# Kernel tuning notes

Measured on AMD Instinct MI355X. Metric: run time of the kernel, lower is better.

The kernel has to match this reference:

```python
import jax, jax.numpy as jnp
import numpy as np

B, N, R, T, E, H, FE = 2, 512, 64, 128, 64, 8, 4
D = E // H  # head_dim = 8


def _layernorm(x, g, b):
    m = x.mean(-1, keepdims=True)
    v = ((x - m) ** 2).mean(-1, keepdims=True)
    return (x - m) / jnp.sqrt(v + 1e-5) * g + b


def _sattn(v, k, q, Wv, Wk, Wq, Wo, bo, mask):
    # v,k: (Bk,Nk,T,E); q: (Bq,Nq,T,E) with Bq possibly 1 (broadcast on batch)
    Bk, Nk, Tk, _ = v.shape
    Nq = q.shape[1]
    v = v.reshape(Bk, Nk, Tk, H, D) @ Wv
    k = k.reshape(Bk, Nk, Tk, H, D) @ Wk
    q = q.reshape(q.shape[0], Nq, Tk, H, D) @ Wq
    q = jnp.broadcast_to(q, (Bk, Nq, Tk, H, D))
    energy = jnp.einsum('bqthd,bkthd->bqkth', q, k)  # (B,Nq,Nk,T,H)
    if mask is not None:
        m = mask[None, :, :, None, None]
        energy = energy * m + (-1e8) * (1.0 - m)
    # note: non-standard softmax over the QUERY axis (dim=1), after scale+clamp
    att = jax.nn.softmax(jnp.clip(energy * (float(E) ** -0.5), -5.0, 5.0), axis=1)
    out = jnp.einsum('bqkth,bkthd->bqthd', att, v).reshape(Bk, Nq, Tk, E)
    return out @ Wo + bo, att


def setup_inputs() -> dict:
    rng = jax.random.key(0)
    ks = jax.random.split(rng, 40)
    s = 0.05
    inp = {
        'value': jax.random.normal(ks[0], (B, N, T, E), jnp.float32),
        'key': jax.random.normal(ks[1], (B, N, T, E), jnp.float32),
        'query': jax.random.normal(ks[2], (B, N, T, E), jnp.float32),
        'adj_sr': jax.random.randint(ks[3], (N, R), 0, 2).astype(jnp.int32),
        'adj_r': jax.random.randint(ks[4], (R, R), 0, 2).astype(jnp.int32),
        'D_S': jax.random.normal(ks[5], (N, R), jnp.float32) * s,
        'W_emb': jax.random.normal(ks[6], (R, E), jnp.float32) * s,
        'b_emb': jnp.zeros((E,), jnp.float32),
        'I_param': jax.random.normal(ks[7], (R, 1, E), jnp.float32) * s,
        'g1': jnp.ones((E,), jnp.float32), 'beta1': jnp.zeros((E,), jnp.float32),
        'g2': jnp.ones((E,), jnp.float32), 'beta2': jnp.zeros((E,), jnp.float32),
        'W_ff1': jax.random.normal(ks[8], (E, FE * E), jnp.float32) * s,
        'b_ff1': jnp.zeros((FE * E,), jnp.float32),
        'W_ff2': jax.random.normal(ks[9], (FE * E, E), jnp.float32) * s,
        'b_ff2': jnp.zeros((E,), jnp.float32),
        'W_fs': jax.random.normal(ks[10], (E, E), jnp.float32) * s,
        'b_fs': jnp.zeros((E,), jnp.float32),
    }
    i = 11
    for tag in ('sr', 'rr', 'rs'):
        inp['Wv_' + tag] = jax.random.normal(ks[i + 0], (D, D), jnp.float32) * s
        inp['Wk_' + tag] = jax.random.normal(ks[i + 1], (D, D), jnp.float32) * s
        inp['Wq_' + tag] = jax.random.normal(ks[i + 2], (D, D), jnp.float32) * s
        inp['Wo_' + tag] = jax.random.normal(ks[i + 3], (E, E), jnp.float32) * s
        inp['bo_' + tag] = jnp.zeros((E,), jnp.float32)
        i += 4
    return inp


def reference(value, key, query, adj_sr, adj_r, D_S, W_emb, b_emb, I_param,
              g1, beta1, g2, beta2, W_ff1, b_ff1, W_ff2, b_ff2, W_fs, b_fs,
              Wv_sr, Wk_sr, Wq_sr, Wo_sr, bo_sr,
              Wv_rr, Wk_rr, Wq_rr, Wo_rr, bo_rr,
              Wv_rs, Wk_rs, Wq_rs, Wo_rs, bo_rs):
    m_sr = adj_sr.T.astype(jnp.float32)  # (R,N)
    m_r = adj_r.astype(jnp.float32)      # (R,R)
    ds = D_S @ W_emb + b_emb             # (N,E)
    q = query + ds[None, :, None, :]
    k = key + ds[None, :, None, :]
    v = value
    Iq = jnp.broadcast_to(I_param[None], (1, R, T, E))  # I.repeat(1,1,T,1)
    Hh, asr = _sattn(v, k, Iq, Wv_sr, Wk_sr, Wq_sr, Wo_sr, bo_sr, m_sr)
    Hh, arr = _sattn(Hh, Hh, Hh, Wv_rr, Wk_rr, Wq_rr, Wo_rr, bo_rr, m_r)
    attn, ars = _sattn(Hh, Hh, q, Wv_rs, Wk_rs, Wq_rs, Wo_rs, bo_rs, None)
    x = _layernorm(attn + q, g1, beta1)          # dropout=0.0 -> identity
    ff = jax.nn.relu(x @ W_ff1 + b_ff1) @ W_ff2 + b_ff2
    U = _layernorm(ff + x, g2, beta2)
    out = U @ W_fs + b_fs
    return (out, asr, arr, ars, Hh)
```

## Files before the change

### kernel.cpp

```cpp
#include <hip/hip_runtime.h>
#include <hip/hip_bf16.h>

typedef __hip_bfloat16 bf16;

#define Bc 2
#define Nc 512
#define Rc 64
#define Tc 128
#define Ec 64
#define Hc 8
#define THc 1024
#define FFc 256

__device__ __forceinline__ bf16  f2b(float x){ return __float2bfloat16(x); }
__device__ __forceinline__ float us2f(unsigned short u){
  union { unsigned int i; float f; } c; c.i = ((unsigned int)u) << 16; return c.f;
}
__device__ __forceinline__ float clip5(float x){ return fminf(fmaxf(x, -5.0f), 5.0f); }

__device__ __forceinline__ float wave_sum64(float v){
#pragma unroll
  for (int o = 32; o > 0; o >>= 1) v += __shfl_xor(v, o, 64);
  return v;
}
__device__ __forceinline__ void wave_sum64x2(float& a, float& b){
#pragma unroll
  for (int o = 32; o > 0; o >>= 1){
    a += __shfl_xor(a, o, 64);
    b += __shfl_xor(b, o, 64);
  }
}
__device__ __forceinline__ void wave_sum64x4(float& a, float& b, float& c, float& d){
#pragma unroll
  for (int o = 32; o > 0; o >>= 1){
    a += __shfl_xor(a, o, 64);
    b += __shfl_xor(b, o, 64);
    c += __shfl_xor(c, o, 64);
    d += __shfl_xor(d, o, 64);
  }
}

__device__ __forceinline__ float rowred16_sum(float v){
  v += __shfl_xor(v, 1, 64);
  v += __shfl_xor(v, 2, 64);
  v += __shfl_xor(v, 4, 64);
  v += __shfl_xor(v, 8, 64);
  return v;
}

__global__ __launch_bounds__(64) void k_prep(
    const float* __restrict__ DS, const float* __restrict__ Wemb,
    const float* __restrict__ bemb, const float* __restrict__ Ip,
    const float* __restrict__ Wq, float* __restrict__ ds, float* __restrict__ qhat)
{
  int bid = blockIdx.x, t = threadIdx.x;
  if (bid < Nc){
    int n = bid, e = t;
    __shared__ float row[Rc];
    row[t] = DS[n*Rc + t];
    __syncthreads();
    float acc = bemb[e];
    for (int r = 0; r < Rc; ++r) acc += row[r] * Wemb[r*Ec + e];
    ds[n*Ec + e] = acc;
  } else {
    int r = bid - Nc;
    __shared__ float irow[Ec];
    irow[t] = Ip[r*Ec + t];
    __syncthreads();
    int h = t >> 3, d = t & 7;
    float acc = 0.0f;
#pragma unroll
    for (int d0 = 0; d0 < 8; ++d0) acc += irow[h*8 + d0] * Wq[d0*8 + d];
    qhat[r*Ec + h*8 + d] = acc;
  }
}

__global__ __launch_bounds__(256) void k_proj_sr(
    const float* __restrict__ key, const float* __restrict__ value,
    const float* __restrict__ ds, const float* __restrict__ Wk,
    const float* __restrict__ Wv, float* __restrict__ khat, float* __restrict__ vhat)
{
  __shared__ float wk[64], wv[64];
  int t = threadIdx.x;
  if (t < 64){ wk[t] = Wk[t]; wv[t] = Wv[t]; }
  __syncthreads();
  int u = blockIdx.x*256 + t;
  int h = u & 7;
  int nt = u >> 3;
  int n = (nt / Tc) % Nc;
  const float* kp = key + (size_t)u*8;
  const float* vp = value + (size_t)u*8;
  const float* dsp = ds + n*Ec + h*8;
  float kin[8], vin[8];
#pragma unroll
  for (int d = 0; d < 8; ++d){ kin[d] = kp[d] + dsp[d]; vin[d] = vp[d]; }
  float* ko = khat + (size_t)u*8;
  float* vo = vhat + (size_t)u*8;
#pragma unroll
  for (int d = 0; d < 8; ++d){
    float ka = 0.0f, va = 0.0f;
#pragma unroll
    for (int d0 = 0; d0 < 8; ++d0){ ka += kin[d0]*wk[d0*8+d]; va += vin[d0]*wv[d0*8+d]; }
    ko[d] = ka; vo[d] = va;
  }
}

__global__ __launch_bounds__(256) void k_asr_write(
    const float* __restrict__ khat, const float* __restrict__ qhat,
    const int* __restrict__ adj_sr, float* __restrict__ o_asr,
    float* __restrict__ rDsr)
{
  __shared__ float ql[4096];
  const float EXPM5 = 0.006737946999085467f;
  int bid = blockIdx.x;
  int b = bid >> 8, np = bid & 255;
  int tid = threadIdx.x;
  int n = np*2 + (tid >> 7);
  int t = tid & 127;
#pragma unroll
  for (int i = 0; i < 16; ++i) ql[i*256 + tid] = qhat[i*256 + tid];
  __syncthreads();
  const float* kp = khat + ((size_t)((b*Nc + n)*Tc + t))*Ec;
  float kr[64];
#pragma unroll
  for (int i = 0; i < 16; ++i) *(float4*)&kr[i*4] = *(const float4*)&kp[i*4];

  float s[8] = {0,0,0,0,0,0,0,0};
  for (int r = 0; r < 64; ++r){
    int m = adj_sr[n*Rc + r];
    if (m){
      const float* qr = &ql[r*64];
#pragma unroll
      for (int h = 0; h < 8; ++h){
        float4 qa = *(const float4*)&qr[h*8];
        float4 qb = *(const float4*)&qr[h*8 + 4];
        float e = qa.x*kr[h*8+0] + qa.y*kr[h*8+1] + qa.z*kr[h*8+2] + qa.w*kr[h*8+3]
                + qb.x*kr[h*8+4] + qb.y*kr[h*8+5] + qb.z*kr[h*8+6] + qb.w*kr[h*8+7];
        s[h] += __expf(clip5(e*0.125f));
      }
    } else {
#pragma unroll
      for (int h = 0; h < 8; ++h) s[h] += EXPM5;
    }
  }
  float rs_[8];
#pragma unroll
  for (int h = 0; h < 8; ++h) rs_[h] = __builtin_amdgcn_rcpf(s[h]);
  {
    size_t dbase = ((size_t)((b*Nc + n)*Tc + t))*8;
    *(float4*)&rDsr[dbase]     = make_float4(rs_[0], rs_[1], rs_[2], rs_[3]);
    *(float4*)&rDsr[dbase + 4] = make_float4(rs_[4], rs_[5], rs_[6], rs_[7]);
  }

  for (int r = 0; r < 64; ++r){
    int m = adj_sr[n*Rc + r];
    float a[8];
    if (m){
      const float* qr = &ql[r*64];
#pragma unroll
      for (int h = 0; h < 8; ++h){
        float4 qa = *(const float4*)&qr[h*8];
        float4 qb = *(const float4*)&qr[h*8 + 4];
        float e = qa.x*kr[h*8+0] + qa.y*kr[h*8+1] + qa.z*kr[h*8+2] + qa.w*kr[h*8+3]
                + qb.x*kr[h*8+4] + qb.y*kr[h*8+5] + qb.z*kr[h*8+6] + qb.w*kr[h*8+7];
        a[h] = __expf(clip5(e*0.125f)) * rs_[h];
      }
    } else {
#pragma unroll
      for (int h = 0; h < 8; ++h) a[h] = EXPM5 * rs_[h];
    }
    size_t ao = ((size_t)((b*Rc + r)*Nc + n))*THc + t*8;
    *(float4*)&o_asr[ao]     = make_float4(a[0], a[1], a[2], a[3]);
    *(float4*)&o_asr[ao + 4] = make_float4(a[4], a[5], a[6], a[7]);
  }
}

__global__ __launch_bounds__(256) void k_attn_sr(
    const float* __restrict__ khat, const float* __restrict__ vhat,
    const float* __restrict__ qhat, const int* __restrict__ adj_sr,
    const float* __restrict__ rD, float* __restrict__ pre)
{
  __shared__ float accs[4][64][8];
  __shared__ float rDl[512];
  int bid = blockIdx.x;
  int b = bid >> 10, th = bid & 1023;
  int t = th >> 3, h = th & 7;
  int tid = threadIdx.x;
  int r = tid & 63, w = tid >> 6;
  rDl[tid]       = rD[((size_t)((b*Nc + tid      )*Tc + t))*8 + h];
  rDl[tid + 256] = rD[((size_t)((b*Nc + tid + 256)*Tc + t))*8 + h];
  float q[8];
#pragma unroll
  for (int d = 0; d < 8; ++d) q[d] = qhat[r*Ec + h*8 + d];
  __syncthreads();
  float acc[8] = {0,0,0,0,0,0,0,0};
  int n0 = w*128;
  for (int n = n0; n < n0 + 128; n += 2){
    size_t goA = ((size_t)((b*Nc + n)*Tc + t))*Ec + h*8;
    size_t goB = goA + (size_t)Tc*Ec;
    const float* kA = khat + goA;
    const float* kB = khat + goB;
    float eA = 0.0f, eB = 0.0f;
#pragma unroll
    for (int d = 0; d < 8; ++d){ eA += q[d]*kA[d]; eB += q[d]*kB[d]; }
    int mA = adj_sr[n*Rc + r], mB = adj_sr[(n+1)*Rc + r];
    eA = mA ? clip5(eA*0.125f) : -5.0f;
    eB = mB ? clip5(eB*0.125f) : -5.0f;
    float aA = __expf(eA) * rDl[n];
    float aB = __expf(eB) * rDl[n+1];
    const float* vA = vhat + goA;
    const float* vB = vhat + goB;
#pragma unroll
    for (int d = 0; d < 8; ++d) acc[d] += aA*vA[d] + aB*vB[d];
  }
#pragma unroll
  for (int d = 0; d < 8; ++d) accs[w][r][d] = acc[d];
  __syncthreads();
  if (w == 0){
    size_t po = ((size_t)((b*Rc + r)*Tc + t))*Ec + h*8;
#pragma unroll
    for (int d = 0; d < 8; ++d)
      pre[po + d] = accs[0][r][d] + accs[1][r][d] + accs[2][r][d] + accs[3][r][d];
  }
}

__global__ __launch_bounds__(256) void k_attn_rr(
    const float* __restrict__ qh, const float* __restrict__ kh,
    const float* __restrict__ vh, const int* __restrict__ adj_r,
    bf16* __restrict__ att_c, float* __restrict__ pre)
{
  __shared__ float accs[4][64][8];
  int bid = blockIdx.x;
  int b = bid >> 10, th = bid & 1023;
  int t = th >> 3, h = th & 7;
  int tid = threadIdx.x;
  int q = tid & 63, w = tid >> 6;
  size_t qo = ((size_t)((b*Rc + q)*Tc + t))*Ec + h*8;
  float qv[8];
#pragma unroll
  for (int d = 0; d < 8; ++d) qv[d] = qh[qo + d];
  float acc[8] = {0,0,0,0,0,0,0,0};
  int k0 = w*16;
  for (int k = k0; k < k0 + 16; k += 2){
    size_t koA = ((size_t)((b*Rc + k)*Tc + t))*Ec + h*8;
    size_t koB = koA + (size_t)Tc*Ec;
    const float* kA = kh + koA;
    const float* kB = kh + koB;
    float eA = 0.0f, eB = 0.0f;
#pragma unroll
    for (int d = 0; d < 8; ++d){ eA += qv[d]*kA[d]; eB += qv[d]*kB[d]; }
    int mA = adj_r[q*Rc + k], mB = adj_r[q*Rc + k + 1];
    eA = mA ? clip5(eA*0.125f) : -5.0f;
    eB = mB ? clip5(eB*0.125f) : -5.0f;
    float pA = __expf(eA), pB = __expf(eB);
    float sA = pA, sB = pB;
    wave_sum64x2(sA, sB);
    float aA = pA/sA, aB = pB/sB;
    size_t ao = ((size_t)(b*Rc + k)*THc + th)*Rc + q;
    att_c[ao] = f2b(aA);
    att_c[ao + (size_t)THc*Rc] = f2b(aB);
    const float* vA = vh + koA;
    const float* vB = vh + koB;
#pragma unroll
    for (int d = 0; d < 8; ++d) acc[d] += aA*vA[d] + aB*vB[d];
  }
#pragma unroll
  for (int d = 0; d < 8; ++d) accs[w][q][d] = acc[d];
  __syncthreads();
  if (w == 0){
#pragma unroll
    for (int d = 0; d < 8; ++d)
      pre[qo + d] = accs[0][q][d] + accs[1][q][d] + accs[2][q][d] + accs[3][q][d];
  }
}

__global__ __launch_bounds__(512) void k_attn_rs(
    const float* __restrict__ query, const float* __restrict__ ds,
    const float* __restrict__ Wq, const float* __restrict__ kh,
    const float* __restrict__ vh, bf16* __restrict__ att_c, float* __restrict__ pre)
{
  __shared__ float wq[64];
  __shared__ float kl[64][8];
  __shared__ float vl[64][8];
  __shared__ float part[8][64];
  __shared__ float redr[64];
  int bid = blockIdx.x;
  int b = bid >> 10, th = bid & 1023;
  int t = th >> 3, h = th & 7;
  int q = threadIdx.x;
  if (q < 64) wq[q] = Wq[q];
  {
    int kk = q >> 3, d = q & 7;
    size_t o = ((size_t)((b*Rc + kk)*Tc + t))*Ec + h*8 + d;
    kl[kk][d] = kh[o];
    vl[kk][d] = vh[o];
  }
  __syncthreads();
  size_t qro = ((size_t)((b*Nc + q)*Tc + t))*Ec + h*8;
  const float* dsp = ds + q*Ec + h*8;
  float xin[8], qv[8];
#pragma unroll
  for (int d = 0; d < 8; ++d) xin[d] = query[qro + d] + dsp[d];
#pragma unroll
  for (int d = 0; d < 8; ++d){
    float a = 0.0f;
#pragma unroll
    for (int d0 = 0; d0 < 8; ++d0) a += xin[d0]*wq[d0*8 + d];
    qv[d] = a;
  }
  int lane = q & 63, wv = q >> 6;
  for (int k = 0; k < 64; k += 4){
    float s0 = 0.0f, s1 = 0.0f, s2 = 0.0f, s3 = 0.0f;
#pragma unroll
    for (int d = 0; d < 8; ++d){
      s0 += qv[d]*kl[k  ][d];
      s1 += qv[d]*kl[k+1][d];
      s2 += qv[d]*kl[k+2][d];
      s3 += qv[d]*kl[k+3][d];
    }
    s0 = __expf(clip5(s0*0.125f));
    s1 = __expf(clip5(s1*0.125f));
    s2 = __expf(clip5(s2*0.125f));
    s3 = __expf(clip5(s3*0.125f));
    wave_sum64x4(s0, s1, s2, s3);
    if (lane == 0){
      part[wv][k] = s0; part[wv][k+1] = s1; part[wv][k+2] = s2; part[wv][k+3] = s3;
    }
  }
  __syncthreads();
  if (q < 64){
    float s = 0.0f;
#pragma unroll
    for (int w2 = 0; w2 < 8; ++w2) s += part[w2][q];
    redr[q] = __builtin_amdgcn_rcpf(s);
  }
  __syncthreads();
  float acc[8] = {0,0,0,0,0,0,0,0};
  for (int k = 0; k < 64; k += 2){
    float eA = 0.0f, eB = 0.0f;
#pragma unroll
    for (int d = 0; d < 8; ++d){ eA += qv[d]*kl[k][d]; eB += qv[d]*kl[k+1][d]; }
    float aA = __expf(clip5(eA*0.125f)) * redr[k];
    float aB = __expf(clip5(eB*0.125f)) * redr[k+1];
    size_t ao = ((size_t)(b*Rc + k)*THc + th)*Nc + q;
    att_c[ao] = f2b(aA);
    att_c[ao + (size_t)THc*Nc] = f2b(aB);
#pragma unroll
    for (int d = 0; d < 8; ++d) acc[d] += aA*vl[k][d] + aB*vl[k+1][d];
  }
#pragma unroll
  for (int d = 0; d < 8; ++d) pre[qro + d] = acc[d];
}

__global__ __launch_bounds__(256) void k_transpose(
    const unsigned short* __restrict__ src, float* __restrict__ dst,
    int W, int C)
{
  __shared__ unsigned short tile[64][66];
  int bid = blockIdx.x;
  int nct = C >> 6;
  int ct = bid % nct; bid /= nct;
  int tht = bid & 15; bid >>= 4;
  int w = bid % W; int b = bid / W;
  int tt = threadIdx.x;
  {
    int cs = tt & 63, i0 = tt >> 6;
    const unsigned short* sb = src + ((size_t)(b*W + w)*THc + tht*64)*C + ct*64;
#pragma unroll
    for (int p = 0; p < 16; ++p){
      int i = i0 + p*4;
      tile[i][cs] = sb[(size_t)i*C + cs];
    }
  }
  __syncthreads();
  {
    int i = tt & 63, c0 = tt >> 6;
#pragma unroll
    for (int p = 0; p < 16; ++p){
      int cs = c0 + p*4;
      int c = ct*64 + cs;
      dst[((size_t)(b*C + c)*W + w)*THc + tht*64 + i] = us2f(tile[i][cs]);
    }
  }
}

__global__ __launch_bounds__(256) void k_wo(
    const float* __restrict__ pre, int nparts, int pstride,
    const float* __restrict__ Wo,
    const float* __restrict__ bo, float* __restrict__ outf,
    float* __restrict__ outf2, int nrows)
{
  int gt = blockIdx.x*256 + threadIdx.x;
  int row = gt >> 6, lane = gt & 63;
  if (row >= nrows) return;
  float xin = 0.0f;
  for (int p2 = 0; p2 < nparts; ++p2)
    xin += pre[(size_t)p2*pstride + (size_t)row*64 + lane];
  float acc = bo[lane];
  for (int e = 0; e < 64; ++e){
    float xe = __shfl(xin, e, 64);
    acc += xe * Wo[e*64 + lane];
  }
  outf[(size_t)row*64 + lane] = acc;
  if (outf2) outf2[(size_t)row*64 + lane] = acc;
}

__global__ __launch_bounds__(256) void k_proj3(
    const float* __restrict__ src, const float* Wq, const float* Wk, const float* Wv,
    float* qh, float* kh, float* vh, int nunits)
{
  __shared__ float wq[64], wk[64], wv[64];
  int t = threadIdx.x;
  if (t < 64){
    wq[t] = Wq ? Wq[t] : 0.0f;
    wk[t] = Wk[t];
    wv[t] = Wv[t];
  }
  __syncthreads();
  int u = blockIdx.x*256 + t;
  if (u >= nunits) return;
  const float* sp = src + (size_t)u*8;
  float xin[8];
#pragma unroll
  for (int d = 0; d < 8; ++d) xin[d] = sp[d];
#pragma unroll
  for (int d = 0; d < 8; ++d){
    float qa = 0.0f, ka = 0.0f, va = 0.0f;
#pragma unroll
    for (int d0 = 0; d0 < 8; ++d0){
      qa += xin[d0]*wq[d0*8 + d];
      ka += xin[d0]*wk[d0*8 + d];
      va += xin[d0]*wv[d0*8 + d];
    }
    if (qh) qh[(size_t)u*8 + d] = qa;
    kh[(size_t)u*8 + d] = ka;
    vh[(size_t)u*8 + d] = va;
  }
}

__device__ __forceinline__ void gemm64x64(
    const float (* __restrict__ Xs)[68], const float* __restrict__ W,
    int Wld, int r0, int c0, float acc[4][4])
{
#pragma unroll 4
  for (int k = 0; k < 64; k += 4){
    float4 xr0 = *(const float4*)&Xs[r0+0][k];
    float4 xr1 = *(const float4*)&Xs[r0+1][k];
    float4 xr2 = *(const float4*)&Xs[r0+2][k];
    float4 xr3 = *(const float4*)&Xs[r0+3][k];
#pragma unroll
    for (int kk = 0; kk < 4; ++kk){
      float4 w = *(const float4*)&W[(size_t)(k+kk)*Wld + c0];
      float x0 = (&xr0.x)[kk], x1 = (&xr1.x)[kk];
      float x2 = (&xr2.x)[kk], x3 = (&xr3.x)[kk];
      acc[0][0] += x0*w.x; acc[0][1] += x0*w.y; acc[0][2] += x0*w.z; acc[0][3] += x0*w.w;
      acc[1][0] += x1*w.x; acc[1][1] += x1*w.y; acc[1][2] += x1*w.z; acc[1][3] += x1*w.w;
      acc[2][0] += x2*w.x; acc[2][1] += x2*w.y; acc[2][2] += x2*w.z; acc[2][3] += x2*w.w;
      acc[3][0] += x3*w.x; acc[3][1] += x3*w.y; acc[3][2] += x3*w.z; acc[3][3] += x3*w.w;
    }
  }
}

__device__ __forceinline__ void ln64(
    const float acc[4][4], float4 g, float4 b, float out[4][4])
{
#pragma unroll
  for (int i = 0; i < 4; ++i){
    float s = acc[i][0] + acc[i][1] + acc[i][2] + acc[i][3];
    float m = rowred16_sum(s) * (1.0f/64.0f);
    float d0 = acc[i][0] - m, d1 = acc[i][1] - m, d2 = acc[i][2] - m, d3 = acc[i][3] - m;
    float vv = d0*d0 + d1*d1 + d2*d2 + d3*d3;
    float var = rowred16_sum(vv) * (1.0f/64.0f);
    float rs = rsqrtf(var + 1e-5f);
    out[i][0] = d0*rs*g.x + b.x;
    out[i][1] = d1*rs*g.y + b.y;
    out[i][2] = d2*rs*g.z + b.z;
    out[i][3] = d3*rs*g.w + b.w;
  }
}

__global__ __launch_bounds__(256) void k_tail(
    const float* __restrict__ pre3, const float* __restrict__ query,
    const float* __restrict__ ds,
    const float* __restrict__ Wo, const float* __restrict__ bo,
    const float* __restrict__ g1, const float* __restrict__ be1,
    const float* __restrict__ W1, const float* __restrict__ b1,
    const float* __restrict__ W2, const float* __restrict__ b2,
    const float* __restrict__ g2, const float* __restrict__ be2,
    const float* __restrict__ Wfs, const float* __restrict__ bfs,
    float* __restrict__ outp)
{
  __shared__ float Xs[64][68];
  __shared__ float Hs[64][68];
  int tid = threadIdx.x;
  int cg = tid & 15, rg = tid >> 4;
  int r0 = rg*4, c0 = cg*4;
  int row_base = blockIdx.x * 64;
  int n = (row_base >> 7) & (Nc - 1);

#pragma unroll
  for (int i = 0; i < 4; ++i){
    float4 t = *(const float4*)&pre3[(size_t)(row_base + r0 + i)*64 + c0];
    *(float4*)&Xs[r0+i][c0] = t;
  }

  float4 bo4  = *(const float4*)&bo[c0];
  float4 ds4  = *(const float4*)&ds[n*64 + c0];
  float4 g14  = *(const float4*)&g1[c0];
  float4 be14 = *(const float4*)&be1[c0];
  float4 b24  = *(const float4*)&b2[c0];
  float4 g24  = *(const float4*)&g2[c0];
  float4 be24 = *(const float4*)&be2[c0];
  float4 bfs4 = *(const float4*)&bfs[c0];
  __syncthreads();

  float acc[4][4];
#pragma unroll
  for (int i = 0; i < 4; ++i){
    acc[i][0] = bo4.x; acc[i][1] = bo4.y; acc[i][2] = bo4.z; acc[i][3] = bo4.w;
  }
  gemm64x64(Xs, Wo, 64, r0, c0, acc);
#pragma unroll
  for (int i = 0; i < 4; ++i){
    float4 qv = *(const float4*)&query[(size_t)(row_base + r0 + i)*64 + c0];
    acc[i][0] += qv.x + ds4.x;
    acc[i][1] += qv.y + ds4.y;
    acc[i][2] += qv.z + ds4.z;
    acc[i][3] += qv.w + ds4.w;
  }
  float xt[4][4];
  ln64(acc, g14, be14, xt);
  __syncthreads();
#pragma unroll
  for (int i = 0; i < 4; ++i)
    *(float4*)&Xs[r0+i][c0] = make_float4(xt[i][0], xt[i][1], xt[i][2], xt[i][3]);
  __syncthreads();

  float ff[4][4];
#pragma unroll
  for (int i = 0; i < 4; ++i){
    ff[i][0] = b24.x; ff[i][1] = b24.y; ff[i][2] = b24.z; ff[i][3] = b24.w;
  }
  for (int p = 0; p < 4; ++p){
    float4 b14 = *(const float4*)&b1[p*64 + c0];
    float h[4][4];
#pragma unroll
    for (int i = 0; i < 4; ++i){
      h[i][0] = b14.x; h[i][1] = b14.y; h[i][2] = b14.z; h[i][3] = b14.w;
    }
    gemm64x64(Xs, W1 + p*64, 256, r0, c0, h);
#pragma unroll
    for (int i = 0; i < 4; ++i){
      h[i][0] = fmaxf(h[i][0], 0.0f); h[i][1] = fmaxf(h[i][1], 0.0f);
      h[i][2] = fmaxf(h[i][2], 0.0f); h[i][3] = fmaxf(h[i][3], 0.0f);
    }
    __syncthreads();
#pragma unroll
    for (int i = 0; i < 4; ++i)
      *(float4*)&Hs[r0+i][c0] = make_float4(h[i][0], h[i][1], h[i][2], h[i][3]);
    __syncthreads();
    gemm64x64(Hs, W2 + (size_t)p*64*64, 64, r0, c0, ff);
  }

#pragma unroll
  for (int i = 0; i < 4; ++i){
    float4 xv = *(const float4*)&Xs[r0+i][c0];
    ff[i][0] += xv.x; ff[i][1] += xv.y; ff[i][2] += xv.z; ff[i][3] += xv.w;
  }
  float U[4][4];
  ln64(ff, g24, be24, U);
  __syncthreads();
#pragma unroll
  for (int i = 0; i < 4; ++i)
    *(float4*)&Hs[r0+i][c0] = make_float4(U[i][0], U[i][1], U[i][2], U[i][3]);
  __syncthreads();

  float o[4][4];
#pragma unroll
  for (int i = 0; i < 4; ++i){
    o[i][0] = bfs4.x; o[i][1] = bfs4.y; o[i][2] = bfs4.z; o[i][3] = bfs4.w;
  }
  gemm64x64(Hs, Wfs, 64, r0, c0, o);
#pragma unroll
  for (int i = 0; i < 4; ++i)
    *(float4*)&outp[(size_t)(row_base + r0 + i)*64 + c0] =
        make_float4(o[i][0], o[i][1], o[i][2], o[i][3]);
}

extern "C" void kernel_launch(void* const* d_in, const int* in_sizes, int n_in,
                              void* d_out, int out_size, void* d_ws, size_t ws_size,
                              hipStream_t stream)
{
  const float* value = (const float*)d_in[0];
  const float* key   = (const float*)d_in[1];
  const float* query = (const float*)d_in[2];
  const int*  adj_sr = (const int*)d_in[3];
  const int*  adj_r  = (const int*)d_in[4];
  const float* D_S   = (const float*)d_in[5];
  const float* W_emb = (const float*)d_in[6];
  const float* b_emb = (const float*)d_in[7];
  const float* I_par = (const float*)d_in[8];
  const float* g1    = (const float*)d_in[9];
  const float* be1   = (const float*)d_in[10];
  const float* g2    = (const float*)d_in[11];
  const float* be2   = (const float*)d_in[12];
  const float* W_ff1 = (const float*)d_in[13];
  const float* b_ff1 = (const float*)d_in[14];
  const float* W_ff2 = (const float*)d_in[15];
  const float* b_ff2 = (const float*)d_in[16];
  const float* W_fs  = (const float*)d_in[17];
  const float* b_fs  = (const float*)d_in[18];
  const float* Wv_sr = (const float*)d_in[19];
  const float* Wk_sr = (const float*)d_in[20];
  const float* Wq_sr = (const float*)d_in[21];
  const float* Wo_sr = (const float*)d_in[22];
  const float* bo_sr = (const float*)d_in[23];
  const float* Wv_rr = (const float*)d_in[24];
  const float* Wk_rr = (const float*)d_in[25];
  const float* Wq_rr = (const float*)d_in[26];
  const float* Wo_rr = (const float*)d_in[27];
  const float* bo_rr = (const float*)d_in[28];
  const float* Wv_rs = (const float*)d_in[29];
  const float* Wk_rs = (const float*)d_in[30];
  const float* Wq_rs = (const float*)d_in[31];
  const float* Wo_rs = (const float*)d_in[32];
  const float* bo_rs = (const float*)d_in[33];

  float* outp  = (float*)d_out;
  float* o_out = outp;
  float* o_asr = outp + 8388608;
  float* o_arr = outp + 75497472;
  float* o_ars = outp + 83886080;
  float* o_hh  = outp + 150994944;

  float* wsf = (float*)d_ws;
  float* ws_ds   = wsf;
  float* ws_qsr  = wsf + 32768;
  bf16*  ws_att  = (bf16*)(wsf + 36864);
  float* ws_rDsr = wsf + 36864;
  float* pool    = wsf + 36864 + 33554432;
  float* ws_ksr  = pool;
  float* ws_vsr  = pool + 8388608;
  float* ws_pre1 = pool + 16777216;
  float* ws_hh1  = pool + 17825792;
  float* ws_qrr  = pool;
  float* ws_krr  = pool + 1048576;
  float* ws_vrr  = pool + 2097152;
  float* ws_pre2 = pool + 3145728;
  float* ws_hh2  = pool + 4194304;
  float* ws_krs  = pool + 5242880;
  float* ws_vrs  = pool + 6291456;
  float* ws_pre3 = pool + 7340032;

  k_prep<<<576, 64, 0, stream>>>(D_S, W_emb, b_emb, I_par, Wq_sr, ws_ds, ws_qsr);
  k_proj_sr<<<4096, 256, 0, stream>>>(key, value, ws_ds, Wk_sr, Wv_sr, ws_ksr, ws_vsr);
  k_asr_write<<<512, 256, 0, stream>>>(ws_ksr, ws_qsr, adj_sr, o_asr, ws_rDsr);
  k_attn_sr<<<2048, 256, 0, stream>>>(ws_ksr, ws_vsr, ws_qsr, adj_sr,
                                      ws_rDsr, ws_pre1);
  k_wo<<<4096, 256, 0, stream>>>(ws_pre1, 1, 0, Wo_sr, bo_sr,
                                 ws_hh1, (float*)nullptr, 16384);

  k_proj3<<<512, 256, 0, stream>>>(ws_hh1, Wq_rr, Wk_rr, Wv_rr,
                                   ws_qrr, ws_krr, ws_vrr, 131072);
  k_attn_rr<<<2048, 256, 0, stream>>>(ws_qrr, ws_krr, ws_vrr, adj_r, ws_att, ws_pre2);
  k_transpose<<<2048, 256, 0, stream>>>((const unsigned short*)ws_att, o_arr, 64, 64);
  k_wo<<<4096, 256, 0, stream>>>(ws_pre2, 1, 0, Wo_rr, bo_rr, ws_hh2, o_hh, 16384);

  k_proj3<<<512, 256, 0, stream>>>(ws_hh2, (const float*)nullptr, Wk_rs, Wv_rs,
                                   (float*)nullptr, ws_krs, ws_vrs, 131072);
  k_attn_rs<<<2048, 512, 0, stream>>>(query, ws_ds, Wq_rs, ws_krs, ws_vrs,
                                      ws_att, ws_pre3);
  k_transpose<<<16384, 256, 0, stream>>>((const unsigned short*)ws_att, o_ars, 64, 512);

  k_tail<<<2048, 256, 0, stream>>>(ws_pre3, query, ws_ds, Wo_rs, bo_rs,
                                   g1, be1, W_ff1, b_ff1, W_ff2, b_ff2,
                                   g2, be2, W_fs, b_fs, o_out);
}
```

Before: 855.2 us.

## Recompute rs attention directly in output layout and tile Wo projection

The rs attention kernel no longer writes a bf16 attention buffer for a later transpose. It saves only the per-key reciprocal softmax denominators, and a new kernel recomputes the query projections and energies and writes the rs attention output directly in the final layout. This removes a large bf16 intermediate write plus a full read-and-transpose pass over it, at the cost of recomputing the exp and dot products. Separately, k_wo becomes a 64-row tiled shared-memory GEMM reusing gemm64x64 instead of one wave per row broadcasting with shuffles.

```diff
diff --git a/kernel.cpp b/kernel.cpp
--- a/kernel.cpp
+++ b/kernel.cpp
@@ -18,11 +18,6 @@
 }
 __device__ __forceinline__ float clip5(float x){ return fminf(fmaxf(x, -5.0f), 5.0f); }
 
-__device__ __forceinline__ float wave_sum64(float v){
-#pragma unroll
-  for (int o = 32; o > 0; o >>= 1) v += __shfl_xor(v, o, 64);
-  return v;
-}
 __device__ __forceinline__ void wave_sum64x2(float& a, float& b){
 #pragma unroll
   for (int o = 32; o > 0; o >>= 1){
@@ -277,7 +272,8 @@
 __global__ __launch_bounds__(512) void k_attn_rs(
     const float* __restrict__ query, const float* __restrict__ ds,
     const float* __restrict__ Wq, const float* __restrict__ kh,
-    const float* __restrict__ vh, bf16* __restrict__ att_c, float* __restrict__ pre)
+    const float* __restrict__ vh, float* __restrict__ rDrs,
+    float* __restrict__ pre)
 {
   __shared__ float wq[64];
   __shared__ float kl[64][8];
@@ -332,7 +328,9 @@
     float s = 0.0f;
 #pragma unroll
     for (int w2 = 0; w2 < 8; ++w2) s += part[w2][q];
-    redr[q] = __builtin_amdgcn_rcpf(s);
+    float r_ = __builtin_amdgcn_rcpf(s);
+    redr[q] = r_;
+    rDrs[((size_t)((b*Rc + q)*Tc + t))*8 + h] = r_;
   }
   __syncthreads();
   float acc[8] = {0,0,0,0,0,0,0,0};
@@ -342,14 +340,59 @@
     for (int d = 0; d < 8; ++d){ eA += qv[d]*kl[k][d]; eB += qv[d]*kl[k+1][d]; }
     float aA = __expf(clip5(eA*0.125f)) * redr[k];
     float aB = __expf(clip5(eB*0.125f)) * redr[k+1];
-    size_t ao = ((size_t)(b*Rc + k)*THc + th)*Nc + q;
-    att_c[ao] = f2b(aA);
-    att_c[ao + (size_t)THc*Nc] = f2b(aB);
 #pragma unroll
     for (int d = 0; d < 8; ++d) acc[d] += aA*vl[k][d] + aB*vl[k+1][d];
   }
 #pragma unroll
   for (int d = 0; d < 8; ++d) pre[qro + d] = acc[d];
+}
+
+__global__ __launch_bounds__(512) void k_ars_write(
+    const float* __restrict__ query, const float* __restrict__ ds,
+    const float* __restrict__ Wq, const float* __restrict__ kh,
+    const float* __restrict__ rD, float* __restrict__ o_ars)
+{
+  __shared__ float wq[64];
+  int bid = blockIdx.x;
+  int tblk = bid & 1; int qg = (bid >> 1) & 63; int b = bid >> 7;
+  int tid = threadIdx.x;
+  int dt = tid >> 3, h = tid & 7;
+  int t = tblk*64 + dt;
+  if (tid < 64) wq[tid] = Wq[tid];
+  __syncthreads();
+  float qv[8][8];
+#pragma unroll
+  for (int qi = 0; qi < 8; ++qi){
+    int q = qg*8 + qi;
+    const float* qp = query + ((size_t)((b*Nc + q)*Tc + t))*Ec + h*8;
+    const float* dp = ds + q*Ec + h*8;
+    float xin[8];
+#pragma unroll
+    for (int d = 0; d < 8; ++d) xin[d] = qp[d] + dp[d];
+#pragma unroll
+    for (int d = 0; d < 8; ++d){
+      float a = 0.0f;
+#pragma unroll
+      for (int d0 = 0; d0 < 8; ++d0) a += xin[d0]*wq[d0*8 + d];
+      qv[qi][d] = a;
+    }
+  }
+  size_t qbase = ((size_t)(b*Nc + qg*8)*Rc)*THc + t*8 + h;
+  for (int k = 0; k < 64; ++k){
+    const float* kp = kh + ((size_t)((b*Rc + k)*Tc + t))*Ec + h*8;
+    float khr[8];
+#pragma unroll
+    for (int d = 0; d < 8; ++d) khr[d] = kp[d];
+    float rd = rD[((size_t)((b*Rc + k)*Tc + t))*8 + h];
+#pragma unroll
+    for (int qi = 0; qi < 8; ++qi){
+      float e = 0.0f;
+#pragma unroll
+      for (int d = 0; d < 8; ++d) e += qv[qi][d]*khr[d];
+      float a = __expf(clip5(e*0.125f)) * rd;
+      o_ars[qbase + (size_t)qi*Rc*THc + (size_t)k*THc] = a;
+    }
+  }
 }
 
 __global__ __launch_bounds__(256) void k_transpose(
@@ -384,60 +427,6 @@
   }
 }
 
-__global__ __launch_bounds__(256) void k_wo(
-    const float* __restrict__ pre, int nparts, int pstride,
-    const float* __restrict__ Wo,
-    const float* __restrict__ bo, float* __restrict__ outf,
-    float* __restrict__ outf2, int nrows)
-{
-  int gt = blockIdx.x*256 + threadIdx.x;
-  int row = gt >> 6, lane = gt & 63;
-  if (row >= nrows) return;
-  float xin = 0.0f;
-  for (int p2 = 0; p2 < nparts; ++p2)
-    xin += pre[(size_t)p2*pstride + (size_t)row*64 + lane];
-  float acc = bo[lane];
-  for (int e = 0; e < 64; ++e){
-    float xe = __shfl(xin, e, 64);
-    acc += xe * Wo[e*64 + lane];
-  }
-  outf[(size_t)row*64 + lane] = acc;
-  if (outf2) outf2[(size_t)row*64 + lane] = acc;
-}
-
-__global__ __launch_bounds__(256) void k_proj3(
-    const float* __restrict__ src, const float* Wq, const float* Wk, const float* Wv,
-    float* qh, float* kh, float* vh, int nunits)
-{
-  __shared__ float wq[64], wk[64], wv[64];
-  int t = threadIdx.x;
-  if (t < 64){
-    wq[t] = Wq ? Wq[t] : 0.0f;
-    wk[t] = Wk[t];
-    wv[t] = Wv[t];
-  }
-  __syncthreads();
-  int u = blockIdx.x*256 + t;
-  if (u >= nunits) return;
-  const float* sp = src + (size_t)u*8;
-  float xin[8];
-#pragma unroll
-  for (int d = 0; d < 8; ++d) xin[d] = sp[d];
-#pragma unroll
-  for (int d = 0; d < 8; ++d){
-    float qa = 0.0f, ka = 0.0f, va = 0.0f;
-#pragma unroll
-    for (int d0 = 0; d0 < 8; ++d0){
-      qa += xin[d0]*wq[d0*8 + d];
-      ka += xin[d0]*wk[d0*8 + d];
-      va += xin[d0]*wv[d0*8 + d];
-    }
-    if (qh) qh[(size_t)u*8 + d] = qa;
-    kh[(size_t)u*8 + d] = ka;
-    vh[(size_t)u*8 + d] = va;
-  }
-}
-
 __device__ __forceinline__ void gemm64x64(
     const float (* __restrict__ Xs)[68], const float* __restrict__ W,
     int Wld, int r0, int c0, float acc[4][4])
@@ -458,6 +447,68 @@
       acc[2][0] += x2*w.x; acc[2][1] += x2*w.y; acc[2][2] += x2*w.z; acc[2][3] += x2*w.w;
       acc[3][0] += x3*w.x; acc[3][1] += x3*w.y; acc[3][2] += x3*w.z; acc[3][3] += x3*w.w;
     }
+  }
+}
+
+__global__ __launch_bounds__(256) void k_wo(
+    const float* __restrict__ pre, const float* __restrict__ Wo,
+    const float* __restrict__ bo, float* __restrict__ outf,
+    float* __restrict__ outf2)
+{
+  __shared__ float Xs[64][68];
+  int tid = threadIdx.x;
+  int cg = tid & 15, rg = tid >> 4;
+  int r0 = rg*4, c0 = cg*4;
+  int row_base = blockIdx.x * 64;
+#pragma unroll
+  for (int i = 0; i < 4; ++i)
+    *(float4*)&Xs[r0+i][c0] = *(const float4*)&pre[(size_t)(row_base + r0 + i)*64 + c0];
+  float4 bo4 = *(const float4*)&bo[c0];
+  __syncthreads();
+  float acc[4][4];
+#pragma unroll
+  for (int i = 0; i < 4; ++i){
+    acc[i][0] = bo4.x; acc[i][1] = bo4.y; acc[i][2] = bo4.z; acc[i][3] = bo4.w;
+  }
+  gemm64x64(Xs, Wo, 64, r0, c0, acc);
+#pragma unroll
+  for (int i = 0; i < 4; ++i){
+    float4 v = make_float4(acc[i][0], acc[i][1], acc[i][2], acc[i][3]);
+    *(float4*)&outf[(size_t)(row_base + r0 + i)*64 + c0] = v;
+    if (outf2) *(float4*)&outf2[(size_t)(row_base + r0 + i)*64 + c0] = v;
+  }
+}
+
+__global__ __launch_bounds__(256) void k_proj3(
+    const float* __restrict__ src, const float* Wq, const float* Wk, const float* Wv,
+    float* qh, float* kh, float* vh, int nunits)
+{
+  __shared__ float wq[64], wk[64], wv[64];
+  int t = threadIdx.x;
+  if (t < 64){
+    wq[t] = Wq ? Wq[t] : 0.0f;
+    wk[t] = Wk[t];
+    wv[t] = Wv[t];
+  }
+  __syncthreads();
+  int u = blockIdx.x*256 + t;
+  if (u >= nunits) return;
+  const float* sp = src + (size_t)u*8;
+  float xin[8];
+#pragma unroll
+  for (int d = 0; d < 8; ++d) xin[d] = sp[d];
+#pragma unroll
+  for (int d = 0; d < 8; ++d){
+    float qa = 0.0f, ka = 0.0f, va = 0.0f;
+#pragma unroll
+    for (int d0 = 0; d0 < 8; ++d0){
+      qa += xin[d0]*wq[d0*8 + d];
+      ka += xin[d0]*wk[d0*8 + d];
+      va += xin[d0]*wv[d0*8 + d];
+    }
+    if (qh) qh[(size_t)u*8 + d] = qa;
+    kh[(size_t)u*8 + d] = ka;
+    vh[(size_t)u*8 + d] = va;
   }
 }
 
@@ -651,26 +702,27 @@
   float* ws_krs  = pool + 5242880;
   float* ws_vrs  = pool + 6291456;
   float* ws_pre3 = pool + 7340032;
+  float* ws_rDrs = pool + 15728640;
 
   k_prep<<<576, 64, 0, stream>>>(D_S, W_emb, b_emb, I_par, Wq_sr, ws_ds, ws_qsr);
   k_proj_sr<<<4096, 256, 0, stream>>>(key, value, ws_ds, Wk_sr, Wv_sr, ws_ksr, ws_vsr);
   k_asr_write<<<512, 256, 0, stream>>>(ws_ksr, ws_qsr, adj_sr, o_asr, ws_rDsr);
   k_attn_sr<<<2048, 256, 0, stream>>>(ws_ksr, ws_vsr, ws_qsr, adj_sr,
                                       ws_rDsr, ws_pre1);
-  k_wo<<<4096, 256, 0, stream>>>(ws_pre1, 1, 0, Wo_sr, bo_sr,
-                                 ws_hh1, (float*)nullptr, 16384);
+  k_wo<<<256, 256, 0, stream>>>(ws_pre1, Wo_sr, bo_sr, ws_hh1, (float*)nullptr);
 
   k_proj3<<<512, 256, 0, stream>>>(ws_hh1, Wq_rr, Wk_rr, Wv_rr,
                                    ws_qrr, ws_krr, ws_vrr, 131072);
   k_attn_rr<<<2048, 256, 0, stream>>>(ws_qrr, ws_krr, ws_vrr, adj_r, ws_att, ws_pre2);
   k_transpose<<<2048, 256, 0, stream>>>((const unsigned short*)ws_att, o_arr, 64, 64);
-  k_wo<<<4096, 256, 0, stream>>>(ws_pre2, 1, 0, Wo_rr, bo_rr, ws_hh2, o_hh, 16384);
+  k_wo<<<256, 256, 0, stream>>>(ws_pre2, Wo_rr, bo_rr, ws_hh2, o_hh);
 
   k_proj3<<<512, 256, 0, stream>>>(ws_hh2, (const float*)nullptr, Wk_rs, Wv_rs,
                                    (float*)nullptr, ws_krs, ws_vrs, 131072);
   k_attn_rs<<<2048, 512, 0, stream>>>(query, ws_ds, Wq_rs, ws_krs, ws_vrs,
-                                      ws_att, ws_pre3);
-  k_transpose<<<16384, 256, 0, stream>>>((const unsigned short*)ws_att, o_ars, 64, 512);
+                                      ws_rDrs, ws_pre3);
+  k_ars_write<<<256, 512, 0, stream>>>(query, ws_ds, Wq_rs, ws_krs,
+                                       ws_rDrs, o_ars);
 
   k_tail<<<2048, 256, 0, stream>>>(ws_pre3, query, ws_ds, Wo_rs, bo_rs,
                                    g1, be1, W_ff1, b_ff1, W_ff2, b_ff2,
```

Measured after the change: 816.2 us. -4.6%, faster.
